# Performance work log

Measured on AMD Instinct MI355X. Metric: run time of the kernel, lower is better.

## Reference

```python
import jax, jax.numpy as jnp
import numpy as np

N_NODES = 50000
N_EDGES = 800000
HEADS = 8
CH = 64


def setup_inputs() -> dict:
    key = jax.random.key(0)
    ks = jax.random.split(key, 30)
    rn = lambda k, shape, s=0.1: (jax.random.normal(k, shape, jnp.float32) * s)
    inp = {
        'x': jax.random.normal(ks[0], (N_NODES, 3), jnp.float32),
        'edge_index': jax.random.randint(ks[1], (2, N_EDGES), 0, N_NODES, jnp.int32),
        'edge_attr': jax.random.normal(ks[2], (N_EDGES, 1), jnp.float32),
        'return_attention_weights': 1,
        # node / residual encoders
        'Wn': rn(ks[3], (3, 64)), 'bn': jnp.zeros((64,), jnp.float32),
        'Wr': rn(ks[4], (3, 512)), 'br': jnp.zeros((512,), jnp.float32),
        'W1': rn(ks[5], (64, 512)), 'as1': rn(ks[6], (HEADS, CH)), 'ad1': rn(ks[7], (HEADS, CH)), 'bc1': jnp.zeros((512,), jnp.float32),
        'W2': rn(ks[8], (512, 512)), 'as2': rn(ks[9], (HEADS, CH)), 'ad2': rn(ks[10], (HEADS, CH)), 'bc2': jnp.zeros((512,), jnp.float32),
        'W3': rn(ks[11], (512, 512)), 'as3': rn(ks[12], (HEADS, CH)), 'ad3': rn(ks[13], (HEADS, CH)), 'bc3': jnp.zeros((64,), jnp.float32),
        # node head
        'Wo': rn(ks[14], (64, 2)), 'bo': jnp.zeros((2,), jnp.float32),
        # edge classifier MLP 136 -> 256 -> 2
        'Wm1': rn(ks[15], (136, 256)), 'bm1': jnp.zeros((256,), jnp.float32),
        'Wm2': rn(ks[16], (256, 2)), 'bm2': jnp.zeros((2,), jnp.float32),
    }
    return inp


def _gat(h, src, dst, W, a_src, a_dst, b, concat):
    """PyG GATConv (shared lin, edge_dim=None, eval-mode dropout)."""
    n = h.shape[0]
    g = (h @ W).reshape(n, HEADS, CH)                      # [N,H,C]
    asrc = jnp.sum(g * a_src[None], -1)                    # [N,H]
    adst = jnp.sum(g * a_dst[None], -1)                    # [N,H]
    e = jax.nn.leaky_relu(asrc[src] + adst[dst], 0.2)      # [E',H]
    m = jax.ops.segment_max(e, dst, num_segments=n)        # softmax per destination
    ex = jnp.exp(e - m[dst])
    s = jax.ops.segment_sum(ex, dst, num_segments=n)
    alpha = ex / s[dst]                                    # [E',H]
    out = jax.ops.segment_sum(g[src] * alpha[..., None], dst, num_segments=n)  # [N,H,C]
    out = out.reshape(n, HEADS * CH) if concat else out.mean(axis=1)
    return out + b, alpha


def reference(x, edge_index, edge_attr, return_attention_weights,
              Wn, bn, Wr, br,
              W1, as1, ad1, bc1,
              W2, as2, ad2, bc2,
              W3, as3, ad3, bc3,
              Wo, bo, Wm1, bm1, Wm2, bm2):
    n = x.shape[0]
    e_len = edge_attr.shape[0]
    src0, dst0 = edge_index[0], edge_index[1]
    # GATConv adds self loops internally
    loop = jnp.arange(n, dtype=edge_index.dtype)
    src = jnp.concatenate([src0, loop])
    dst = jnp.concatenate([dst0, loop])

    h = x @ Wn + bn          # node_encoder (dropout is eval identity)
    res = x @ Wr + br        # self.linear residual
    # edge_encoder output is unused by GATConv (edge_dim=None) -> no-op

    o, _ = _gat(h, src, dst, W1, as1, ad1, bc1, concat=True)
    o = jax.nn.elu(o) + res
    o, _ = _gat(o, src, dst, W2, as2, ad2, bc2, concat=True)
    o = jax.nn.elu(o) + res
    o, alpha = _gat(o, src, dst, W3, as3, ad3, bc3, concat=False)
    node_embedding = jax.nn.elu(o)                          # [N,64]

    x_out = node_embedding @ Wo + bo                        # [N,2]
    edge_embedding = jnp.concatenate(
        [node_embedding[src0], alpha[:e_len], node_embedding[dst0]], axis=-1)  # [E,136]
    edge_out = jax.nn.relu(edge_embedding @ Wm1 + bm1) @ Wm2 + bm2             # [E,2]
    return x_out, edge_out
```

## Files before the change

### kernel.cpp

```cpp
#include <hip/hip_runtime.h>
#include <hip/hip_bf16.h>
#include <math.h>

#define N_NODES 50000
#define NPAD    50048
#define N_EDGES 800000
#define EPRIME  (N_EDGES + N_NODES)
#define HEADS 8
#define CH 64
#define FDIM 512

typedef unsigned short ushort_t;
typedef __attribute__((ext_vector_type(8))) short bf16x8_t;
typedef __attribute__((ext_vector_type(4))) float f32x4_t;

__device__ __forceinline__ float bf2f(unsigned short u) {
  union { unsigned int i; float f; } v; v.i = ((unsigned int)u) << 16; return v.f;
}
__device__ __forceinline__ unsigned short f2bf(float f) {
  union { float f; unsigned int i; } v; v.f = f;
  unsigned int x = v.i;
  return (unsigned short)((x + 0x7fffu + ((x >> 16) & 1u)) >> 16);
}
__device__ __forceinline__ float ldf(const void* p, size_t idx, int isf32) {
  return isf32 ? ((const float*)p)[idx] : bf2f(((const ushort_t*)p)[idx]);
}
__device__ __forceinline__ void stf(void* p, size_t idx, float v, int isf32) {
  if (isf32) ((float*)p)[idx] = v;
  else       ((ushort_t*)p)[idx] = f2bf(v);
}
__device__ __forceinline__ float leakyf(float v) { return v >= 0.f ? v : 0.2f * v; }
__device__ __forceinline__ float eluf(float v)   { return v > 0.f ? v : expm1f(v); }

typedef const __attribute__((address_space(1))) unsigned int* gas1_t;
typedef __attribute__((address_space(3))) unsigned int* las3_t;
__device__ __forceinline__ void gll16(const ushort_t* g, ushort_t* l) {
  __builtin_amdgcn_global_load_lds((gas1_t)g, (las3_t)l, 16, 0, 0);
}

__global__ void detect_dtype(const void* Wn, int* flag) {
  if (blockIdx.x == 0 && threadIdx.x == 0) {
    const ushort_t* u = (const ushort_t*)Wn;
    int extreme = 0;
    for (int i = 0; i < 384; ++i) {
      float v = fabsf(bf2f(u[i]));
      if (v != 0.f && (v > 16.f || v < 6.1e-5f)) extreme++;
    }
    *flag = (extreme >= 20) ? 1 : 0;
  }
}

__global__ void convert_wt(const void* __restrict__ src, ushort_t* __restrict__ dst,
                           int K, int N, int boff, const int* __restrict__ dflag) {
  int isf32 = *dflag;
  int tid = blockIdx.x * blockDim.x + threadIdx.x;
  if (tid >= N * K) return;
  int n = tid / K, k = tid % K;
  dst[tid] = f2bf(ldf(src, (size_t)(boff + k) * N + n, isf32));
}

__global__ void convert_att(const void* s1, const void* d1, const void* s2, const void* d2,
                            const void* s3, const void* d3, ushort_t* __restrict__ dst,
                            const int* __restrict__ dflag) {
  int isf32 = *dflag;
  int tid = blockIdx.x * blockDim.x + threadIdx.x;
  if (tid >= 6 * 512) return;
  int which = tid >> 9, idx = tid & 511;
  const void* p = which == 0 ? s1 : which == 1 ? d1 : which == 2 ? s2
                : which == 3 ? d2 : which == 4 ? s3 : d3;
  dst[tid] = f2bf(ldf(p, idx, isf32));
}

__global__ void init_deg(int* deg, int* fill) {
  int n = blockIdx.x * blockDim.x + threadIdx.x;
  if (n < N_NODES) { deg[n] = 1; fill[n] = 0; }
}

__global__ void count_edges(const int* __restrict__ ei, int* deg) {
  int e = blockIdx.x * blockDim.x + threadIdx.x;
  if (e < N_EDGES) atomicAdd(&deg[ei[N_EDGES + e]], 1);
}

__global__ void scan64(const int* __restrict__ deg, int* __restrict__ rowptr) {
  const int CHUNK = (N_NODES + 63) / 64;
  int t = threadIdx.x;
  int lo = t * CHUNK;
  int hi = lo + CHUNK; if (hi > N_NODES) hi = N_NODES;
  int s = 0;
  for (int i = lo; i < hi; ++i) s += deg[i];
  int inc = s;
  #pragma unroll
  for (int off = 1; off < 64; off <<= 1) {
    int u = __shfl_up(inc, off);
    if (t >= off) inc += u;
  }
  int run = inc - s;
  for (int i = lo; i < hi; ++i) { rowptr[i] = run; run += deg[i]; }
  if (t == 63) rowptr[N_NODES] = run;
}

__global__ void fill_csr(const int* __restrict__ ei, const int* __restrict__ rowptr,
                         int* fill, int* __restrict__ csr_src) {
  int e = blockIdx.x * blockDim.x + threadIdx.x;
  if (e >= EPRIME) return;
  int s, d;
  if (e < N_EDGES) { s = ei[e]; d = ei[N_EDGES + e]; }
  else             { s = d = e - N_EDGES; }
  int pos = rowptr[d] + atomicAdd(&fill[d], 1);
  csr_src[pos] = s;
}

__global__ void encode_h(const void* __restrict__ x, const void* __restrict__ Wn,
                         const void* __restrict__ bn, ushort_t* __restrict__ h,
                         const int* __restrict__ dflag) {
  int isf32 = *dflag;
  int tid = blockIdx.x * blockDim.x + threadIdx.x;
  if (tid >= N_NODES * 64) return;
  int n = tid >> 6, j = tid & 63;
  float x0 = ldf(x, n * 3 + 0, isf32), x1 = ldf(x, n * 3 + 1, isf32), x2 = ldf(x, n * 3 + 2, isf32);
  float v = x0 * ldf(Wn, j, isf32) + x1 * ldf(Wn, 64 + j, isf32)
          + x2 * ldf(Wn, 128 + j, isf32) + ldf(bn, j, isf32);
  h[tid] = f2bf(v);
}

__global__ __launch_bounds__(256) void gemm_bt(
    const ushort_t* __restrict__ A, const ushort_t* __restrict__ BT,
    ushort_t* __restrict__ C, int K, int ldc,
    const ushort_t* __restrict__ att, float* __restrict__ asrc, float* __restrict__ adst)
{
  __shared__ __align__(16) ushort_t As[128][32];
  __shared__ __align__(16) ushort_t Bs[128][32];
  int tid = threadIdx.x;
  int wave = tid >> 6, lane = tid & 63;
  int wr = wave >> 1, wc = wave & 1;
  int row0 = blockIdx.x * 128, col0 = blockIdx.y * 128;
  int fm = lane & 15, fq = lane >> 4;

  f32x4_t acc[4][4];
  #pragma unroll
  for (int i = 0; i < 4; ++i)
    #pragma unroll
    for (int j = 0; j < 4; ++j) acc[i][j] = (f32x4_t){0.f, 0.f, 0.f, 0.f};

  int srow = wave * 32 + (lane >> 2);
  int skel = (lane & 3) * 8;
  const ushort_t* aG0 = A  + (size_t)(row0 + srow) * K + skel;
  const ushort_t* aG1 = A  + (size_t)(row0 + srow + 16) * K + skel;
  const ushort_t* bG0 = BT + (size_t)(col0 + srow) * K + skel;
  const ushort_t* bG1 = BT + (size_t)(col0 + srow + 16) * K + skel;
  ushort_t* aL0 = &As[wave * 32][0];
  ushort_t* aL1 = &As[wave * 32 + 16][0];
  ushort_t* bL0 = &Bs[wave * 32][0];
  ushort_t* bL1 = &Bs[wave * 32 + 16][0];

  for (int k0 = 0; k0 < K; k0 += 32) {
    gll16(aG0 + k0, aL0);
    gll16(aG1 + k0, aL1);
    gll16(bG0 + k0, bL0);
    gll16(bG1 + k0, bL1);
    __syncthreads();
    bf16x8_t af[4], bfr[4];
    #pragma unroll
    for (int i = 0; i < 4; ++i) af[i]  = *(const bf16x8_t*)&As[64 * wr + 16 * i + fm][fq * 8];
    #pragma unroll
    for (int j = 0; j < 4; ++j) bfr[j] = *(const bf16x8_t*)&Bs[64 * wc + 16 * j + fm][fq * 8];
    #pragma unroll
    for (int i = 0; i < 4; ++i)
      #pragma unroll
      for (int j = 0; j < 4; ++j)
        acc[i][j] = __builtin_amdgcn_mfma_f32_16x16x32_bf16(af[i], bfr[j], acc[i][j], 0, 0, 0);
    __syncthreads();
  }

  int do_att = (att != nullptr);
  int head = 2 * blockIdx.y + wc;
  float sa[4], sd[4];
  if (do_att) {
    #pragma unroll
    for (int j = 0; j < 4; ++j) {
      int ch = 16 * j + fm;
      sa[j] = bf2f(att[head * CH + ch]);
      sd[j] = bf2f(att[512 + head * CH + ch]);
    }
  }

  #pragma unroll
  for (int i = 0; i < 4; ++i) {
    int rowb = row0 + 64 * wr + 16 * i + fq * 4;
    #pragma unroll
    for (int r = 0; r < 4; ++r) {
      int row = rowb + r;
      float ss = 0.f, dd = 0.f;
      #pragma unroll
      for (int j = 0; j < 4; ++j) {
        ushort_t uv = f2bf(acc[i][j][r]);
        C[(size_t)row * ldc + col0 + 64 * wc + 16 * j + fm] = uv;
        if (do_att) {
          float cv = bf2f(uv);
          ss += cv * sa[j];
          dd += cv * sd[j];
        }
      }
      if (do_att) {
        #pragma unroll
        for (int off = 8; off > 0; off >>= 1) {
          ss += __shfl_down(ss, off);
          dd += __shfl_down(dd, off);
        }
        if (fm == 0 && row < N_NODES) {
          asrc[row * HEADS + head] = ss;
          adst[row * HEADS + head] = dd;
        }
      }
    }
  }
}

__global__ __launch_bounds__(256) void aggregate(
    const int* __restrict__ rowptr, const int* __restrict__ csr_src,
    const float* __restrict__ asrc, const float* __restrict__ adst,
    float* __restrict__ sumv,
    const ushort_t* __restrict__ g,
    const void* __restrict__ x, const void* __restrict__ Wr,
    const void* __restrict__ br, const void* __restrict__ bc,
    ushort_t* __restrict__ out, int mean_mode,
    const void* __restrict__ Wo, const void* __restrict__ bo,
    void* __restrict__ outh, const int* __restrict__ dflag)
{
  int isf32 = *dflag;
  __shared__ float sx[3];
  int n = blockIdx.x;
  int t = threadIdx.x;
  if (t < 3) sx[t] = ldf(x, n * 3 + t, isf32);
  __syncthreads();

  int start = rowptr[n], end = rowptr[n + 1];
  int c0 = t * 2;
  int h  = t >> 5;
  int i0 = n * HEADS + h;
  float ad = adst[i0];

  float l = 0.f, a0 = 0.f, a1 = 0.f;
  int i = start;
  for (; i + 8 <= end; i += 8) {
    int s[8];
    #pragma unroll
    for (int k = 0; k < 8; ++k) s[k] = csr_src[i + k];
    float e[8];
    unsigned int gv[8];
    #pragma unroll
    for (int k = 0; k < 8; ++k) {
      e[k]  = asrc[s[k] * HEADS + h] + ad;
      gv[k] = *(const unsigned int*)(g + (size_t)s[k] * FDIM + c0);
    }
    #pragma unroll
    for (int k = 0; k < 8; ++k) {
      float p = __expf(leakyf(e[k]));
      l  += p;
      a0 += p * bf2f((ushort_t)(gv[k] & 0xffffu));
      a1 += p * bf2f((ushort_t)(gv[k] >> 16));
    }
  }
  for (; i + 2 <= end; i += 2) {
    int s0 = csr_src[i], s1 = csr_src[i + 1];
    float e0 = asrc[s0 * HEADS + h] + ad;
    float e1 = asrc[s1 * HEADS + h] + ad;
    unsigned int g0 = *(const unsigned int*)(g + (size_t)s0 * FDIM + c0);
    unsigned int g1 = *(const unsigned int*)(g + (size_t)s1 * FDIM + c0);
    float p0 = __expf(leakyf(e0)), p1 = __expf(leakyf(e1));
    l  += p0 + p1;
    a0 += p0 * bf2f((ushort_t)(g0 & 0xffffu)) + p1 * bf2f((ushort_t)(g1 & 0xffffu));
    a1 += p0 * bf2f((ushort_t)(g0 >> 16))     + p1 * bf2f((ushort_t)(g1 >> 16));
  }
  if (i < end) {
    int s0 = csr_src[i];
    float p0 = __expf(leakyf(asrc[s0 * HEADS + h] + ad));
    unsigned int g0 = *(const unsigned int*)(g + (size_t)s0 * FDIM + c0);
    l  += p0;
    a0 += p0 * bf2f((ushort_t)(g0 & 0xffffu));
    a1 += p0 * bf2f((ushort_t)(g0 >> 16));
  }
  a0 /= l;
  a1 /= l;
  if ((t & 31) == 0) sumv[i0] = l;

  if (!mean_mode) {
    float r0 = sx[0] * ldf(Wr, c0, isf32)         + sx[1] * ldf(Wr, 512 + c0, isf32)
             + sx[2] * ldf(Wr, 1024 + c0, isf32)  + ldf(br, c0, isf32);
    float r1 = sx[0] * ldf(Wr, c0 + 1, isf32)     + sx[1] * ldf(Wr, 512 + c0 + 1, isf32)
             + sx[2] * ldf(Wr, 1024 + c0 + 1, isf32) + ldf(br, c0 + 1, isf32);
    unsigned int o0 = f2bf(eluf(a0 + ldf(bc, c0, isf32)) + r0);
    unsigned int o1 = f2bf(eluf(a1 + ldf(bc, c0 + 1, isf32)) + r1);
    *(unsigned int*)(out + (size_t)n * FDIM + c0) = o0 | (o1 << 16);
  } else {
    __shared__ float red[512];
    red[c0] = a0; red[c0 + 1] = a1;
    __syncthreads();
    if (t < 64) {
      float tot = 0.f;
      #pragma unroll
      for (int hh = 0; hh < 8; ++hh) tot += red[t + 64 * hh];
      ushort_t uv = f2bf(eluf(tot * 0.125f + ldf(bc, t, isf32)));
      out[(size_t)n * CH + t] = uv;
      float nv = bf2f(uv);
      float p0 = nv * ldf(Wo, t * 2 + 0, isf32);
      float p1 = nv * ldf(Wo, t * 2 + 1, isf32);
      float vv = (t & 1) ? p1 : p0;
      float ww = (t & 1) ? p0 : p1;
      vv += __shfl_xor(ww, 1);
      #pragma unroll
      for (int off = 2; off < 64; off <<= 1) vv += __shfl_xor(vv, off);
      if (t < 2) stf(outh, (size_t)n * 2 + t, vv + ldf(bo, t, isf32), isf32);
    }
  }
}

#define EPW 32
__global__ __launch_bounds__(256) void edge_head3(
    const int* __restrict__ ei, const float* __restrict__ asrc, const float* __restrict__ adst,
    const float* __restrict__ sumv,
    const ushort_t* __restrict__ pq, const void* __restrict__ Wm1,
    const void* __restrict__ bm1, const void* __restrict__ Wm2,
    const void* __restrict__ bm2, void* __restrict__ out,
    const int* __restrict__ dflag)
{
  int isf32 = *dflag;
  int lane = threadIdx.x & 63;
  int c0 = lane * 4;
  float w1r[8][4], w2a[4], w2b[4], b1r[4];
  #pragma unroll
  for (int hh = 0; hh < 8; ++hh)
    #pragma unroll
    for (int j = 0; j < 4; ++j)
      w1r[hh][j] = ldf(Wm1, (64 + hh) * 256 + c0 + j, isf32);
  #pragma unroll
  for (int j = 0; j < 4; ++j) {
    w2a[j] = ldf(Wm2, (c0 + j) * 2 + 0, isf32);
    w2b[j] = ldf(Wm2, (c0 + j) * 2 + 1, isf32);
    b1r[j] = ldf(bm1, c0 + j, isf32);
  }
  float bo0 = ldf(bm2, 0, isf32), bo1 = ldf(bm2, 1, isf32);

  int wid = blockIdx.x * 4 + (threadIdx.x >> 6);
  int e0 = wid * EPW;
  int h = lane & 7;
  for (int e = e0; e < e0 + EPW; e += 2) {
    int sA = ei[e],     dA = ei[N_EDGES + e];
    int sB = ei[e + 1], dB = ei[N_EDGES + e + 1];
    float vA = asrc[sA * HEADS + h] + adst[dA * HEADS + h];
    float vB = asrc[sB * HEADS + h] + adst[dB * HEADS + h];
    float lA = sumv[dA * HEADS + h], lB = sumv[dB * HEADS + h];
    ushort4 pvA = *(const ushort4*)(pq + (size_t)sA * FDIM + c0);
    ushort4 qvA = *(const ushort4*)(pq + (size_t)dA * FDIM + 256 + c0);
    ushort4 pvB = *(const ushort4*)(pq + (size_t)sB * FDIM + c0);
    ushort4 qvB = *(const ushort4*)(pq + (size_t)dB * FDIM + 256 + c0);
    float aA = __expf(leakyf(vA)) / lA;
    float aB = __expf(leakyf(vB)) / lB;
    float alA[8], alB[8];
    #pragma unroll
    for (int hh = 0; hh < 8; ++hh) { alA[hh] = __shfl(aA, hh); alB[hh] = __shfl(aB, hh); }

    float accA0 = 0.f, accA1 = 0.f, accB0 = 0.f, accB1 = 0.f;
    float pA[4] = { bf2f(pvA.x), bf2f(pvA.y), bf2f(pvA.z), bf2f(pvA.w) };
    float qA[4] = { bf2f(qvA.x), bf2f(qvA.y), bf2f(qvA.z), bf2f(qvA.w) };
    float pB[4] = { bf2f(pvB.x), bf2f(pvB.y), bf2f(pvB.z), bf2f(pvB.w) };
    float qB[4] = { bf2f(qvB.x), bf2f(qvB.y), bf2f(qvB.z), bf2f(qvB.w) };
    #pragma unroll
    for (int j = 0; j < 4; ++j) {
      float hvA = pA[j] + qA[j] + b1r[j];
      float hvB = pB[j] + qB[j] + b1r[j];
      #pragma unroll
      for (int hh = 0; hh < 8; ++hh) {
        hvA += alA[hh] * w1r[hh][j];
        hvB += alB[hh] * w1r[hh][j];
      }
      hvA = fmaxf(hvA, 0.f);
      hvB = fmaxf(hvB, 0.f);
      accA0 += hvA * w2a[j]; accA1 += hvA * w2b[j];
      accB0 += hvB * w2a[j]; accB1 += hvB * w2b[j];
    }
    #pragma unroll
    for (int off = 32; off > 0; off >>= 1) {
      accA0 += __shfl_down(accA0, off);
      accA1 += __shfl_down(accA1, off);
      accB0 += __shfl_down(accB0, off);
      accB1 += __shfl_down(accB1, off);
    }
    if (lane == 0) {
      stf(out, 100000 + (size_t)e * 2 + 0, accA0 + bo0, isf32);
      stf(out, 100000 + (size_t)e * 2 + 1, accA1 + bo1, isf32);
      stf(out, 100000 + (size_t)e * 2 + 2, accB0 + bo0, isf32);
      stf(out, 100000 + (size_t)e * 2 + 3, accB1 + bo1, isf32);
    }
  }
}

extern "C" void kernel_launch(void* const* d_in, const int* in_sizes, int n_in,
                              void* d_out, int out_size, void* d_ws, size_t ws_size,
                              hipStream_t stream) {
  const void* x   = d_in[0];
  const int*  ei  = (const int*)d_in[1];
  const void* Wn  = d_in[4];
  const void* bn  = d_in[5];
  const void* Wr  = d_in[6];
  const void* br  = d_in[7];
  const void* W1  = d_in[8];
  const void* as1 = d_in[9];
  const void* ad1 = d_in[10];
  const void* bc1 = d_in[11];
  const void* W2  = d_in[12];
  const void* as2 = d_in[13];
  const void* ad2 = d_in[14];
  const void* bc2 = d_in[15];
  const void* W3  = d_in[16];
  const void* as3 = d_in[17];
  const void* ad3 = d_in[18];
  const void* bc3 = d_in[19];
  const void* Wo  = d_in[20];
  const void* bo  = d_in[21];
  const void* Wm1 = d_in[22];
  const void* bm1 = d_in[23];
  const void* Wm2 = d_in[24];
  const void* bm2 = d_in[25];

  char* ws = (char*)d_ws;
  size_t off = 0;
  auto take = [&](size_t bytes) -> char* {
    char* p = ws + off;
    off += (bytes + 255) & ~(size_t)255;
    return p;
  };
  ushort_t* h_bf   = (ushort_t*)take((size_t)NPAD * 64 * 2);
  ushort_t* g_bf   = (ushort_t*)take((size_t)NPAD * FDIM * 2);
  ushort_t* o_bf   = (ushort_t*)take((size_t)NPAD * FDIM * 2);
  float*    asrc   = (float*)take((size_t)N_NODES * HEADS * 4);
  float*    adst   = (float*)take((size_t)N_NODES * HEADS * 4);
  float*    sumv   = (float*)take((size_t)N_NODES * HEADS * 4);
  int*      rowptr = (int*)take((size_t)(N_NODES + 1) * 4);
  int*      csr_src= (int*)take((size_t)EPRIME * 4);
  int*      deg    = (int*)take((size_t)N_NODES * 4);
  int*      fillc  = (int*)take((size_t)N_NODES * 4);
  int*      dflag  = (int*)take(256);
  ushort_t* WT1    = (ushort_t*)take((size_t)512 * 64 * 2);
  ushort_t* WT2    = (ushort_t*)take((size_t)512 * 512 * 2);
  ushort_t* WT3    = (ushort_t*)take((size_t)512 * 512 * 2);
  ushort_t* WTPQ   = (ushort_t*)take((size_t)512 * 64 * 2);
  ushort_t* attv   = (ushort_t*)take((size_t)6 * 512 * 2);

  dim3 b256(256);
  const int MB = NPAD / 128;

  detect_dtype<<<dim3(1), dim3(64), 0, stream>>>(Wn, dflag);

  convert_wt<<<dim3(128),  b256, 0, stream>>>(W1, WT1, 64, 512, 0, dflag);
  convert_wt<<<dim3(1024), b256, 0, stream>>>(W2, WT2, 512, 512, 0, dflag);
  convert_wt<<<dim3(1024), b256, 0, stream>>>(W3, WT3, 512, 512, 0, dflag);
  convert_wt<<<dim3(64),   b256, 0, stream>>>(Wm1, WTPQ,            64, 256, 0,  dflag);
  convert_wt<<<dim3(64),   b256, 0, stream>>>(Wm1, WTPQ + 256 * 64, 64, 256, 72, dflag);
  convert_att<<<dim3(12),  b256, 0, stream>>>(as1, ad1, as2, ad2, as3, ad3, attv, dflag);

  init_deg<<<dim3((N_NODES + 255) / 256), b256, 0, stream>>>(deg, fillc);
  count_edges<<<dim3((N_EDGES + 255) / 256), b256, 0, stream>>>(ei, deg);
  scan64<<<dim3(1), dim3(64), 0, stream>>>(deg, rowptr);
  fill_csr<<<dim3((EPRIME + 255) / 256), b256, 0, stream>>>(ei, rowptr, fillc, csr_src);

  encode_h<<<dim3((N_NODES * 64 + 255) / 256), b256, 0, stream>>>(x, Wn, bn, h_bf, dflag);

  gemm_bt<<<dim3(MB, 4), b256, 0, stream>>>(h_bf, WT1, g_bf, 64, 512,
                                            attv, asrc, adst);
  aggregate<<<dim3(N_NODES), b256, 0, stream>>>(rowptr, csr_src, asrc, adst, sumv,
                                                g_bf, x, Wr, br, bc1, o_bf, 0,
                                                nullptr, nullptr, d_out, dflag);

  gemm_bt<<<dim3(MB, 4), b256, 0, stream>>>(o_bf, WT2, g_bf, 512, 512,
                                            attv + 1024, asrc, adst);
  aggregate<<<dim3(N_NODES), b256, 0, stream>>>(rowptr, csr_src, asrc, adst, sumv,
                                                g_bf, x, Wr, br, bc2, o_bf, 0,
                                                nullptr, nullptr, d_out, dflag);

  gemm_bt<<<dim3(MB, 4), b256, 0, stream>>>(o_bf, WT3, g_bf, 512, 512,
                                            attv + 2048, asrc, adst);
  aggregate<<<dim3(N_NODES), b256, 0, stream>>>(rowptr, csr_src, asrc, adst, sumv,
                                                g_bf, x, Wr, br, bc3, h_bf, 1,
                                                Wo, bo, d_out, dflag);

  gemm_bt<<<dim3(MB, 4), b256, 0, stream>>>(h_bf, WTPQ, g_bf, 64, 512,
                                            nullptr, nullptr, nullptr);
  edge_head3<<<dim3(N_EDGES / (EPW * 4)), b256, 0, stream>>>(ei, asrc, adst, sumv, g_bf,
                                                             Wm1, bm1, Wm2, bm2,
                                                             d_out, dflag);
}
```

Measured before the change: 1.268 ms.

## Reorder edge head by destination CSR to reuse per-node destination data

```diff
diff --git a/kernel.cpp b/kernel.cpp
--- a/kernel.cpp
+++ b/kernel.cpp
@@ -100,14 +100,15 @@
 }
 
 __global__ void fill_csr(const int* __restrict__ ei, const int* __restrict__ rowptr,
-                         int* fill, int* __restrict__ csr_src) {
+                         int* fill, int* __restrict__ csr_src, int* __restrict__ csr_eid) {
   int e = blockIdx.x * blockDim.x + threadIdx.x;
   if (e >= EPRIME) return;
-  int s, d;
-  if (e < N_EDGES) { s = ei[e]; d = ei[N_EDGES + e]; }
-  else             { s = d = e - N_EDGES; }
+  int s, d, id;
+  if (e < N_EDGES) { s = ei[e]; d = ei[N_EDGES + e]; id = e; }
+  else             { s = d = e - N_EDGES; id = -1; }
   int pos = rowptr[d] + atomicAdd(&fill[d], 1);
   csr_src[pos] = s;
+  csr_eid[pos] = id;
 }
 
 __global__ void encode_h(const void* __restrict__ x, const void* __restrict__ Wn,
@@ -315,9 +316,11 @@
   }
 }
 
-#define EPW 32
-__global__ __launch_bounds__(256) void edge_head3(
-    const int* __restrict__ ei, const float* __restrict__ asrc, const float* __restrict__ adst,
+#define DPW 4
+__global__ __launch_bounds__(256) void edge_head4(
+    const int* __restrict__ rowptr, const int* __restrict__ csr_src,
+    const int* __restrict__ csr_eid,
+    const float* __restrict__ asrc, const float* __restrict__ adst,
     const float* __restrict__ sumv,
     const ushort_t* __restrict__ pq, const void* __restrict__ Wm1,
     const void* __restrict__ bm1, const void* __restrict__ Wm2,
@@ -327,6 +330,7 @@
   int isf32 = *dflag;
   int lane = threadIdx.x & 63;
   int c0 = lane * 4;
+  int h = lane & 7;
   float w1r[8][4], w2a[4], w2b[4], b1r[4];
   #pragma unroll
   for (int hh = 0; hh < 8; ++hh)
@@ -342,55 +346,92 @@
   float bo0 = ldf(bm2, 0, isf32), bo1 = ldf(bm2, 1, isf32);
 
   int wid = blockIdx.x * 4 + (threadIdx.x >> 6);
-  int e0 = wid * EPW;
-  int h = lane & 7;
-  for (int e = e0; e < e0 + EPW; e += 2) {
-    int sA = ei[e],     dA = ei[N_EDGES + e];
-    int sB = ei[e + 1], dB = ei[N_EDGES + e + 1];
-    float vA = asrc[sA * HEADS + h] + adst[dA * HEADS + h];
-    float vB = asrc[sB * HEADS + h] + adst[dB * HEADS + h];
-    float lA = sumv[dA * HEADS + h], lB = sumv[dB * HEADS + h];
-    ushort4 pvA = *(const ushort4*)(pq + (size_t)sA * FDIM + c0);
-    ushort4 qvA = *(const ushort4*)(pq + (size_t)dA * FDIM + 256 + c0);
-    ushort4 pvB = *(const ushort4*)(pq + (size_t)sB * FDIM + c0);
-    ushort4 qvB = *(const ushort4*)(pq + (size_t)dB * FDIM + 256 + c0);
-    float aA = __expf(leakyf(vA)) / lA;
-    float aB = __expf(leakyf(vB)) / lB;
-    float alA[8], alB[8];
-    #pragma unroll
-    for (int hh = 0; hh < 8; ++hh) { alA[hh] = __shfl(aA, hh); alB[hh] = __shfl(aB, hh); }
-
-    float accA0 = 0.f, accA1 = 0.f, accB0 = 0.f, accB1 = 0.f;
-    float pA[4] = { bf2f(pvA.x), bf2f(pvA.y), bf2f(pvA.z), bf2f(pvA.w) };
-    float qA[4] = { bf2f(qvA.x), bf2f(qvA.y), bf2f(qvA.z), bf2f(qvA.w) };
-    float pB[4] = { bf2f(pvB.x), bf2f(pvB.y), bf2f(pvB.z), bf2f(pvB.w) };
-    float qB[4] = { bf2f(qvB.x), bf2f(qvB.y), bf2f(qvB.z), bf2f(qvB.w) };
-    #pragma unroll
-    for (int j = 0; j < 4; ++j) {
-      float hvA = pA[j] + qA[j] + b1r[j];
-      float hvB = pB[j] + qB[j] + b1r[j];
-      #pragma unroll
-      for (int hh = 0; hh < 8; ++hh) {
-        hvA += alA[hh] * w1r[hh][j];
-        hvB += alB[hh] * w1r[hh][j];
-      }
-      hvA = fmaxf(hvA, 0.f);
-      hvB = fmaxf(hvB, 0.f);
-      accA0 += hvA * w2a[j]; accA1 += hvA * w2b[j];
-      accB0 += hvB * w2a[j]; accB1 += hvB * w2b[j];
-    }
-    #pragma unroll
-    for (int off = 32; off > 0; off >>= 1) {
-      accA0 += __shfl_down(accA0, off);
-      accA1 += __shfl_down(accA1, off);
-      accB0 += __shfl_down(accB0, off);
-      accB1 += __shfl_down(accB1, off);
-    }
-    if (lane == 0) {
-      stf(out, 100000 + (size_t)e * 2 + 0, accA0 + bo0, isf32);
-      stf(out, 100000 + (size_t)e * 2 + 1, accA1 + bo1, isf32);
-      stf(out, 100000 + (size_t)e * 2 + 2, accB0 + bo0, isf32);
-      stf(out, 100000 + (size_t)e * 2 + 3, accB1 + bo1, isf32);
+  int n0 = wid * DPW;
+  for (int n = n0; n < n0 + DPW; ++n) {
+    int start = rowptr[n], end = rowptr[n + 1];
+    float ad = adst[n * HEADS + h];
+    float rs = 1.f / sumv[n * HEADS + h];
+    ushort4 qv = *(const ushort4*)(pq + (size_t)n * FDIM + 256 + c0);
+    float qb[4] = { bf2f(qv.x) + b1r[0], bf2f(qv.y) + b1r[1],
+                    bf2f(qv.z) + b1r[2], bf2f(qv.w) + b1r[3] };
+
+    int i = start;
+    for (; i + 2 <= end; i += 2) {
+      int sA = csr_src[i],     sB = csr_src[i + 1];
+      int eA = csr_eid[i],     eB = csr_eid[i + 1];
+      float vA = asrc[sA * HEADS + h] + ad;
+      float vB = asrc[sB * HEADS + h] + ad;
+      ushort4 pvA = *(const ushort4*)(pq + (size_t)sA * FDIM + c0);
+      ushort4 pvB = *(const ushort4*)(pq + (size_t)sB * FDIM + c0);
+      float aA = __expf(leakyf(vA)) * rs;
+      float aB = __expf(leakyf(vB)) * rs;
+      float alA[8], alB[8];
+      #pragma unroll
+      for (int hh = 0; hh < 8; ++hh) { alA[hh] = __shfl(aA, hh); alB[hh] = __shfl(aB, hh); }
+
+      float accA0 = 0.f, accA1 = 0.f, accB0 = 0.f, accB1 = 0.f;
+      float pA[4] = { bf2f(pvA.x), bf2f(pvA.y), bf2f(pvA.z), bf2f(pvA.w) };
+      float pB[4] = { bf2f(pvB.x), bf2f(pvB.y), bf2f(pvB.z), bf2f(pvB.w) };
+      #pragma unroll
+      for (int j = 0; j < 4; ++j) {
+        float hvA = pA[j] + qb[j];
+        float hvB = pB[j] + qb[j];
+        #pragma unroll
+        for (int hh = 0; hh < 8; ++hh) {
+          hvA += alA[hh] * w1r[hh][j];
+          hvB += alB[hh] * w1r[hh][j];
+        }
+        hvA = fmaxf(hvA, 0.f);
+        hvB = fmaxf(hvB, 0.f);
+        accA0 += hvA * w2a[j]; accA1 += hvA * w2b[j];
+        accB0 += hvB * w2a[j]; accB1 += hvB * w2b[j];
+      }
+      #pragma unroll
+      for (int off = 32; off > 0; off >>= 1) {
+        accA0 += __shfl_down(accA0, off);
+        accA1 += __shfl_down(accA1, off);
+        accB0 += __shfl_down(accB0, off);
+        accB1 += __shfl_down(accB1, off);
+      }
+      if (lane == 0) {
+        if (eA >= 0) {
+          stf(out, 100000 + (size_t)eA * 2 + 0, accA0 + bo0, isf32);
+          stf(out, 100000 + (size_t)eA * 2 + 1, accA1 + bo1, isf32);
+        }
+        if (eB >= 0) {
+          stf(out, 100000 + (size_t)eB * 2 + 0, accB0 + bo0, isf32);
+          stf(out, 100000 + (size_t)eB * 2 + 1, accB1 + bo1, isf32);
+        }
+      }
+    }
+    if (i < end) {
+      int sA = csr_src[i];
+      int eA = csr_eid[i];
+      float vA = asrc[sA * HEADS + h] + ad;
+      ushort4 pvA = *(const ushort4*)(pq + (size_t)sA * FDIM + c0);
+      float aA = __expf(leakyf(vA)) * rs;
+      float alA[8];
+      #pragma unroll
+      for (int hh = 0; hh < 8; ++hh) alA[hh] = __shfl(aA, hh);
+      float accA0 = 0.f, accA1 = 0.f;
+      float pA[4] = { bf2f(pvA.x), bf2f(pvA.y), bf2f(pvA.z), bf2f(pvA.w) };
+      #pragma unroll
+      for (int j = 0; j < 4; ++j) {
+        float hvA = pA[j] + qb[j];
+        #pragma unroll
+        for (int hh = 0; hh < 8; ++hh) hvA += alA[hh] * w1r[hh][j];
+        hvA = fmaxf(hvA, 0.f);
+        accA0 += hvA * w2a[j]; accA1 += hvA * w2b[j];
+      }
+      #pragma unroll
+      for (int off = 32; off > 0; off >>= 1) {
+        accA0 += __shfl_down(accA0, off);
+        accA1 += __shfl_down(accA1, off);
+      }
+      if (lane == 0 && eA >= 0) {
+        stf(out, 100000 + (size_t)eA * 2 + 0, accA0 + bo0, isf32);
+        stf(out, 100000 + (size_t)eA * 2 + 1, accA1 + bo1, isf32);
+      }
     }
   }
 }
@@ -438,6 +479,7 @@
   float*    sumv   = (float*)take((size_t)N_NODES * HEADS * 4);
   int*      rowptr = (int*)take((size_t)(N_NODES + 1) * 4);
   int*      csr_src= (int*)take((size_t)EPRIME * 4);
+  int*      csr_eid= (int*)take((size_t)EPRIME * 4);
   int*      deg    = (int*)take((size_t)N_NODES * 4);
   int*      fillc  = (int*)take((size_t)N_NODES * 4);
   int*      dflag  = (int*)take(256);
@@ -462,7 +504,7 @@
   init_deg<<<dim3((N_NODES + 255) / 256), b256, 0, stream>>>(deg, fillc);
   count_edges<<<dim3((N_EDGES + 255) / 256), b256, 0, stream>>>(ei, deg);
   scan64<<<dim3(1), dim3(64), 0, stream>>>(deg, rowptr);
-  fill_csr<<<dim3((EPRIME + 255) / 256), b256, 0, stream>>>(ei, rowptr, fillc, csr_src);
+  fill_csr<<<dim3((EPRIME + 255) / 256), b256, 0, stream>>>(ei, rowptr, fillc, csr_src, csr_eid);
 
   encode_h<<<dim3((N_NODES * 64 + 255) / 256), b256, 0, stream>>>(x, Wn, bn, h_bf, dflag);
 
@@ -486,7 +528,8 @@
 
   gemm_bt<<<dim3(MB, 4), b256, 0, stream>>>(h_bf, WTPQ, g_bf, 64, 512,
                                             nullptr, nullptr, nullptr);
-  edge_head3<<<dim3(N_EDGES / (EPW * 4)), b256, 0, stream>>>(ei, asrc, adst, sumv, g_bf,
+  edge_head4<<<dim3(N_NODES / (DPW * 4)), b256, 0, stream>>>(rowptr, csr_src, csr_eid,
+                                                             asrc, adst, sumv, g_bf,
                                                              Wm1, bm1, Wm2, bm2,
                                                              d_out, dflag);
 }
```

After: 1.297 ms. +2.2%, slower.

## Process edge head in destination-sorted CSR order for gather locality

Applied to the files above, without the earlier changes.

```diff
diff --git a/kernel.cpp b/kernel.cpp
--- a/kernel.cpp
+++ b/kernel.cpp
@@ -6,6 +6,7 @@
 #define NPAD    50048
 #define N_EDGES 800000
 #define EPRIME  (N_EDGES + N_NODES)
+#define EPAD    850048
 #define HEADS 8
 #define CH 64
 #define FDIM 512
@@ -100,14 +101,21 @@
 }
 
 __global__ void fill_csr(const int* __restrict__ ei, const int* __restrict__ rowptr,
-                         int* fill, int* __restrict__ csr_src) {
+                         int* fill, int* __restrict__ csr_src,
+                         int* __restrict__ csr_dst, int* __restrict__ csr_eid) {
   int e = blockIdx.x * blockDim.x + threadIdx.x;
-  if (e >= EPRIME) return;
-  int s, d;
-  if (e < N_EDGES) { s = ei[e]; d = ei[N_EDGES + e]; }
-  else             { s = d = e - N_EDGES; }
+  if (e >= EPAD) return;
+  if (e >= EPRIME) {
+    csr_src[e] = 0; csr_dst[e] = 0; csr_eid[e] = -1;
+    return;
+  }
+  int s, d, id;
+  if (e < N_EDGES) { s = ei[e]; d = ei[N_EDGES + e]; id = e; }
+  else             { s = d = e - N_EDGES; id = -1; }
   int pos = rowptr[d] + atomicAdd(&fill[d], 1);
   csr_src[pos] = s;
+  csr_dst[pos] = d;
+  csr_eid[pos] = id;
 }
 
 __global__ void encode_h(const void* __restrict__ x, const void* __restrict__ Wn,
@@ -282,7 +290,7 @@
   }
   a0 /= l;
   a1 /= l;
-  if ((t & 31) == 0) sumv[i0] = l;
+  if ((t & 31) == 0) sumv[i0] = 1.f / l;
 
   if (!mean_mode) {
     float r0 = sx[0] * ldf(Wr, c0, isf32)         + sx[1] * ldf(Wr, 512 + c0, isf32)
@@ -316,9 +324,11 @@
 }
 
 #define EPW 32
-__global__ __launch_bounds__(256) void edge_head3(
-    const int* __restrict__ ei, const float* __restrict__ asrc, const float* __restrict__ adst,
-    const float* __restrict__ sumv,
+__global__ __launch_bounds__(256) void edge_head5(
+    const int* __restrict__ csr_src, const int* __restrict__ csr_dst,
+    const int* __restrict__ csr_eid,
+    const float* __restrict__ asrc, const float* __restrict__ adst,
+    const float* __restrict__ rsumv,
     const ushort_t* __restrict__ pq, const void* __restrict__ Wm1,
     const void* __restrict__ bm1, const void* __restrict__ Wm2,
     const void* __restrict__ bm2, void* __restrict__ out,
@@ -327,6 +337,7 @@
   int isf32 = *dflag;
   int lane = threadIdx.x & 63;
   int c0 = lane * 4;
+  int h = lane & 7;
   float w1r[8][4], w2a[4], w2b[4], b1r[4];
   #pragma unroll
   for (int hh = 0; hh < 8; ++hh)
@@ -343,19 +354,19 @@
 
   int wid = blockIdx.x * 4 + (threadIdx.x >> 6);
   int e0 = wid * EPW;
-  int h = lane & 7;
   for (int e = e0; e < e0 + EPW; e += 2) {
-    int sA = ei[e],     dA = ei[N_EDGES + e];
-    int sB = ei[e + 1], dB = ei[N_EDGES + e + 1];
+    int sA = csr_src[e],     sB = csr_src[e + 1];
+    int dA = csr_dst[e],     dB = csr_dst[e + 1];
+    int eA = csr_eid[e],     eB = csr_eid[e + 1];
     float vA = asrc[sA * HEADS + h] + adst[dA * HEADS + h];
     float vB = asrc[sB * HEADS + h] + adst[dB * HEADS + h];
-    float lA = sumv[dA * HEADS + h], lB = sumv[dB * HEADS + h];
+    float rsA = rsumv[dA * HEADS + h], rsB = rsumv[dB * HEADS + h];
     ushort4 pvA = *(const ushort4*)(pq + (size_t)sA * FDIM + c0);
     ushort4 qvA = *(const ushort4*)(pq + (size_t)dA * FDIM + 256 + c0);
     ushort4 pvB = *(const ushort4*)(pq + (size_t)sB * FDIM + c0);
     ushort4 qvB = *(const ushort4*)(pq + (size_t)dB * FDIM + 256 + c0);
-    float aA = __expf(leakyf(vA)) / lA;
-    float aB = __expf(leakyf(vB)) / lB;
+    float aA = __expf(leakyf(vA)) * rsA;
+    float aB = __expf(leakyf(vB)) * rsB;
     float alA[8], alB[8];
     #pragma unroll
     for (int hh = 0; hh < 8; ++hh) { alA[hh] = __shfl(aA, hh); alB[hh] = __shfl(aB, hh); }
@@ -387,10 +398,14 @@
       accB1 += __shfl_down(accB1, off);
     }
     if (lane == 0) {
-      stf(out, 100000 + (size_t)e * 2 + 0, accA0 + bo0, isf32);
-      stf(out, 100000 + (size_t)e * 2 + 1, accA1 + bo1, isf32);
-      stf(out, 100000 + (size_t)e * 2 + 2, accB0 + bo0, isf32);
-      stf(out, 100000 + (size_t)e * 2 + 3, accB1 + bo1, isf32);
+      if (eA >= 0) {
+        stf(out, 100000 + (size_t)eA * 2 + 0, accA0 + bo0, isf32);
+        stf(out, 100000 + (size_t)eA * 2 + 1, accA1 + bo1, isf32);
+      }
+      if (eB >= 0) {
+        stf(out, 100000 + (size_t)eB * 2 + 0, accB0 + bo0, isf32);
+        stf(out, 100000 + (size_t)eB * 2 + 1, accB1 + bo1, isf32);
+      }
     }
   }
 }
@@ -437,7 +452,9 @@
   float*    adst   = (float*)take((size_t)N_NODES * HEADS * 4);
   float*    sumv   = (float*)take((size_t)N_NODES * HEADS * 4);
   int*      rowptr = (int*)take((size_t)(N_NODES + 1) * 4);
-  int*      csr_src= (int*)take((size_t)EPRIME * 4);
+  int*      csr_src= (int*)take((size_t)EPAD * 4);
+  int*      csr_dst= (int*)take((size_t)EPAD * 4);
+  int*      csr_eid= (int*)take((size_t)EPAD * 4);
   int*      deg    = (int*)take((size_t)N_NODES * 4);
   int*      fillc  = (int*)take((size_t)N_NODES * 4);
   int*      dflag  = (int*)take(256);
@@ -462,7 +479,8 @@
   init_deg<<<dim3((N_NODES + 255) / 256), b256, 0, stream>>>(deg, fillc);
   count_edges<<<dim3((N_EDGES + 255) / 256), b256, 0, stream>>>(ei, deg);
   scan64<<<dim3(1), dim3(64), 0, stream>>>(deg, rowptr);
-  fill_csr<<<dim3((EPRIME + 255) / 256), b256, 0, stream>>>(ei, rowptr, fillc, csr_src);
+  fill_csr<<<dim3((EPAD + 255) / 256), b256, 0, stream>>>(ei, rowptr, fillc,
+                                                          csr_src, csr_dst, csr_eid);
 
   encode_h<<<dim3((N_NODES * 64 + 255) / 256), b256, 0, stream>>>(x, Wn, bn, h_bf, dflag);
 
@@ -486,7 +504,8 @@
 
   gemm_bt<<<dim3(MB, 4), b256, 0, stream>>>(h_bf, WTPQ, g_bf, 64, 512,
                                             nullptr, nullptr, nullptr);
-  edge_head3<<<dim3(N_EDGES / (EPW * 4)), b256, 0, stream>>>(ei, asrc, adst, sumv, g_bf,
-                                                             Wm1, bm1, Wm2, bm2,
-                                                             d_out, dflag);
-}
+  edge_head5<<<dim3(EPAD / (EPW * 4)), b256, 0, stream>>>(csr_src, csr_dst, csr_eid,
+                                                          asrc, adst, sumv, g_bf,
+                                                          Wm1, bm1, Wm2, bm2,
+                                                          d_out, dflag);
+}
```

Measured after the change: 1.320 ms. +4.0%, slower.
